# Performance work log

Hardware: AMD Instinct MI355X
Metric: run time of the kernel (lower is better)

Reference implementation:

```python
import jax, jax.numpy as jnp
import numpy as np

KEY_DIM = 32
NUM_HEADS = 4
B, T, F, D = 32, 64, 128, 64


def _proj_in(x, w, b):
    # x: [B,T,F,D], w: [D,H,K], b: [H,K] -> [B,T,F,H,K]
    return jnp.einsum("btfd,dhk->btfhk", x, w) + b


def _axial_mha(x, wq, bq, wk, bk, wv, bv, wo, bo, axis):
    # Keras MultiHeadAttention with attention_axes=(axis,); dropout inactive at inference.
    scale = 1.0 / np.sqrt(KEY_DIM)
    q = _proj_in(x, wq, bq) * scale
    k = _proj_in(x, wk, bk)
    v = _proj_in(x, wv, bv)
    if axis == 1:  # temporal attention, feature axis acts as batch
        scores = jnp.einsum("bqfhk,bsfhk->bfhqs", q, k)  # [B,F,H,Tq,Tk]
        probs = jax.nn.softmax(scores, axis=-1)
        o = jnp.einsum("bfhqs,bsfhk->bqfhk", probs, v)
    else:  # feature attention, temporal axis acts as batch
        scores = jnp.einsum("btqhk,btshk->bthqs", q, k)  # [B,T,H,Fq,Fk]
        probs = jax.nn.softmax(scores, axis=-1)
        o = jnp.einsum("bthqs,btshk->btqhk", probs, v)
    return jnp.einsum("btfhk,hkd->btfd", o, wo) + bo


def setup_inputs() -> dict:
    key = jax.random.key(0)
    ks = jax.random.split(key, 10)
    std = 0.02
    w = lambda k, shape: (jax.random.normal(k, shape, jnp.float32) * std)
    inp = {"x": jax.random.normal(ks[0], (B, T, F, D), jnp.float32)}
    for i, n in enumerate(["tq", "tk", "tv", "fq", "fk", "fv"]):
        inp[n + "_w"] = w(ks[1 + i], (D, NUM_HEADS, KEY_DIM))
        inp[n + "_b"] = jnp.zeros((NUM_HEADS, KEY_DIM), jnp.float32)
    inp["to_w"] = w(ks[7], (NUM_HEADS, KEY_DIM, D))
    inp["to_b"] = jnp.zeros((D,), jnp.float32)
    inp["fo_w"] = w(ks[8], (NUM_HEADS, KEY_DIM, D))
    inp["fo_b"] = jnp.zeros((D,), jnp.float32)
    return inp


def reference(x, tq_w, tq_b, tk_w, tk_b, tv_w, tv_b, to_w, to_b,
              fq_w, fq_b, fk_w, fk_b, fv_w, fv_b, fo_w, fo_b):
    temporal_out = _axial_mha(x, tq_w, tq_b, tk_w, tk_b, tv_w, tv_b, to_w, to_b, axis=1)
    feature_out = _axial_mha(x, fq_w, fq_b, fk_w, fk_b, fv_w, fv_b, fo_w, fo_b, axis=2)
    return temporal_out + feature_out
```

## Files before the change

kernel.cpp:

```cpp
#include <hip/hip_runtime.h>

typedef unsigned short u16;
typedef unsigned int   u32;
typedef short v8s __attribute__((ext_vector_type(8)));
typedef float v4f __attribute__((ext_vector_type(4)));

#define DEV __device__ __forceinline__
#define MFMA(a,b,c) __builtin_amdgcn_mfma_f32_16x16x32_bf16((a),(b),(c),0,0,0)

constexpr int Bb = 32, Tt = 64, Ff = 128, Dd = 64, Hh = 4, Kk = 32;

DEV u16 f2b(float f) {
    u32 u = __float_as_uint(f);
    return (u16)((u + 0x7fffu + ((u >> 16) & 1u)) >> 16);
}
DEV u32 pk2(float a, float b) {
    u32 x = __float_as_uint(a) + 0x8000u;
    u32 y = __float_as_uint(b) + 0x8000u;
    return (x >> 16) | (y & 0xffff0000u);
}

__global__ __launch_bounds__(256)
void prep_weights(const float* __restrict__ tq, const float* __restrict__ tk,
                  const float* __restrict__ tv, const float* __restrict__ fq,
                  const float* __restrict__ fk, const float* __restrict__ fv,
                  const float* __restrict__ to_, const float* __restrict__ fo,
                  u16* __restrict__ ws)
{
    int idx = blockIdx.x * 256 + threadIdx.x;
    if (idx < 49152) {
        int p = idx >> 13, rem = idx & 8191;
        int h = rem >> 11, ch = (rem >> 6) & 31, d = rem & 63;
        const float* w = (p==0)?tq:(p==1)?tk:(p==2)?tv:(p==3)?fq:(p==4)?fk:fv;
        ws[idx] = f2b(w[d*128 + h*32 + ch]);
    } else {
        int i2 = idx - 49152;
        int path = i2 >> 13, rem = i2 & 8191;
        int h = rem >> 11, d = (rem >> 5) & 63, k2 = rem & 31;
        const float* w = path ? fo : to_;
        ws[idx] = f2b(w[h*2048 + k2*64 + d]);
    }
}

template<int NR, int MODE>
__global__ __launch_bounds__(NR*4)
void axial_mfma(const float* __restrict__ x, const u16* __restrict__ wsw,
                const float* __restrict__ bq, const float* __restrict__ bk,
                const float* __restrict__ bv, const float* __restrict__ bo,
                float* __restrict__ out)
{
    constexpr int W   = NR / 16;
    constexpr int QP  = 40;
    constexpr int NRp = NR + 8;
    constexpr int o_q  = 0;
    constexpr int o_k  = o_q + NR * QP;
    constexpr int o_vt = o_k + NR * QP;
    constexpr int o_p  = o_vt + 32 * NRp;
    constexpr int SMEM = o_p + NR * NRp;
    __shared__ alignas(16) u16 sm[SMEM];

    const int tid  = threadIdx.x;
    const int w    = tid >> 6;
    const int lane = tid & 63;
    const int quad = lane >> 4;
    const int l15  = lane & 15;
    const int bid  = blockIdx.x;

    int base, rstride;
    if (MODE == 0) { int b = bid >> 7, f = bid & 127; base = b*(Tt*Ff*Dd) + f*Dd; rstride = Ff*Dd; }
    else           { base = bid * (Ff*Dd); rstride = Dd; }

    constexpr int PB = (MODE == 0) ? 0 : 3;
    const u16* wql = wsw + (PB+0)*8192;
    const u16* wkl = wsw + (PB+1)*8192;
    const u16* wvl = wsw + (PB+2)*8192;
    const u16* wol = wsw + 49152 + MODE*8192;

    v8s xfrag[2];
#pragma unroll
    for (int ks = 0; ks < 2; ++ks) {
        const float* xp = x + base + (w*16 + l15)*rstride + ks*32 + quad*8;
        float4 a = *reinterpret_cast<const float4*>(xp);
        float4 b = *reinterpret_cast<const float4*>(xp + 4);
        v8s f;
        u32* fu = reinterpret_cast<u32*>(&f);
        fu[0] = pk2(a.x, a.y); fu[1] = pk2(a.z, a.w);
        fu[2] = pk2(b.x, b.y); fu[3] = pk2(b.z, b.w);
        xfrag[ks] = f;
    }

    v4f outAcc[4];
#pragma unroll
    for (int i = 0; i < 4; ++i) outAcc[i] = (v4f){0.f,0.f,0.f,0.f};

    const float scale = 0.17677669529663687f;
    const v4f vzero = (v4f){0.f,0.f,0.f,0.f};

#pragma unroll 1
    for (int h = 0; h < Hh; ++h) {
        __syncthreads();

        {
            const u16* wb = wql + h*2048;
#pragma unroll
            for (int nt = 0; nt < 2; ++nt) {
                v4f acc = vzero;
#pragma unroll
                for (int ks = 0; ks < 2; ++ks) {
                    v8s wf = *reinterpret_cast<const v8s*>(wb + (nt*16+l15)*64 + ks*32 + quad*8);
                    acc = MFMA(wf, xfrag[ks], acc);
                }
                float4 b4 = *reinterpret_cast<const float4*>(bq + h*32 + nt*16 + quad*4);
                u32 lo = pk2((acc[0]+b4.x)*scale, (acc[1]+b4.y)*scale);
                u32 hi = pk2((acc[2]+b4.z)*scale, (acc[3]+b4.w)*scale);
                *reinterpret_cast<uint2*>(&sm[o_q + (w*16+l15)*QP + nt*16 + quad*4]) = make_uint2(lo, hi);
            }
        }
        {
            const u16* wb = wkl + h*2048;
#pragma unroll
            for (int nt = 0; nt < 2; ++nt) {
                v4f acc = vzero;
#pragma unroll
                for (int ks = 0; ks < 2; ++ks) {
                    v8s wf = *reinterpret_cast<const v8s*>(wb + (nt*16+l15)*64 + ks*32 + quad*8);
                    acc = MFMA(wf, xfrag[ks], acc);
                }
                float4 b4 = *reinterpret_cast<const float4*>(bk + h*32 + nt*16 + quad*4);
                u32 lo = pk2(acc[0]+b4.x, acc[1]+b4.y);
                u32 hi = pk2(acc[2]+b4.z, acc[3]+b4.w);
                *reinterpret_cast<uint2*>(&sm[o_k + (w*16+l15)*QP + nt*16 + quad*4]) = make_uint2(lo, hi);
            }
        }
        {
            const u16* wb = wvl + h*2048;
#pragma unroll
            for (int nt = 0; nt < 2; ++nt) {
                v4f acc = vzero;
#pragma unroll
                for (int ks = 0; ks < 2; ++ks) {
                    v8s wf = *reinterpret_cast<const v8s*>(wb + (nt*16+l15)*64 + ks*32 + quad*8);
                    acc = MFMA(xfrag[ks], wf, acc);
                }
                float bias = bv[h*32 + nt*16 + l15];
                u32 lo = pk2(acc[0]+bias, acc[1]+bias);
                u32 hi = pk2(acc[2]+bias, acc[3]+bias);
                int ch = nt*16 + l15;
                *reinterpret_cast<uint2*>(&sm[o_vt + ch*NRp + w*16 + quad*4]) = make_uint2(lo, hi);
            }
        }
        __syncthreads();

        v8s qf = *reinterpret_cast<const v8s*>(&sm[o_q + (w*16+l15)*QP + quad*8]);
        v4f S[W];
#pragma unroll
        for (int ct = 0; ct < W; ++ct) {
            v8s kf = *reinterpret_cast<const v8s*>(&sm[o_k + (ct*16+l15)*QP + quad*8]);
            S[ct] = MFMA(kf, qf, vzero);
        }
        float mm = S[0][0];
#pragma unroll
        for (int ct = 0; ct < W; ++ct)
#pragma unroll
            for (int r = 0; r < 4; ++r) mm = fmaxf(mm, S[ct][r]);
        mm = fmaxf(mm, __shfl_xor(mm, 16));
        mm = fmaxf(mm, __shfl_xor(mm, 32));
        float ss = 0.f;
#pragma unroll
        for (int ct = 0; ct < W; ++ct)
#pragma unroll
            for (int r = 0; r < 4; ++r) { float p = __expf(S[ct][r] - mm); S[ct][r] = p; ss += p; }
        ss += __shfl_xor(ss, 16);
        ss += __shfl_xor(ss, 32);
        float rl = 1.f / ss;
#pragma unroll
        for (int ct = 0; ct < W; ++ct) {
            u32 lo = pk2(S[ct][0]*rl, S[ct][1]*rl);
            u32 hi = pk2(S[ct][2]*rl, S[ct][3]*rl);
            *reinterpret_cast<uint2*>(&sm[o_p + (w*16+l15)*NRp + ct*16 + quad*4]) = make_uint2(lo, hi);
        }

        v4f Oacc[2] = { vzero, vzero };
#pragma unroll
        for (int ks = 0; ks < NR/32; ++ks) {
            v8s pf = *reinterpret_cast<const v8s*>(&sm[o_p + (w*16+l15)*NRp + ks*32 + quad*8]);
#pragma unroll
            for (int nt = 0; nt < 2; ++nt) {
                v8s vf = *reinterpret_cast<const v8s*>(&sm[o_vt + (nt*16+l15)*NRp + ks*32 + quad*8]);
                Oacc[nt] = MFMA(vf, pf, Oacc[nt]);
            }
        }
#pragma unroll
        for (int nt = 0; nt < 2; ++nt) {
            u32 lo = pk2(Oacc[nt][0], Oacc[nt][1]);
            u32 hi = pk2(Oacc[nt][2], Oacc[nt][3]);
            *reinterpret_cast<uint2*>(&sm[o_q + (w*16+l15)*QP + nt*16 + quad*4]) = make_uint2(lo, hi);
        }

        v8s of = *reinterpret_cast<const v8s*>(&sm[o_q + (w*16+l15)*QP + quad*8]);
        {
            const u16* wb = wol + h*2048;
#pragma unroll
            for (int nt = 0; nt < 4; ++nt) {
                v8s wf = *reinterpret_cast<const v8s*>(wb + (nt*16+l15)*32 + quad*8);
                outAcc[nt] = MFMA(wf, of, outAcc[nt]);
            }
        }
    }

    float* orow = out + base + (w*16 + l15)*rstride;
#pragma unroll
    for (int nt = 0; nt < 4; ++nt) {
        int d0 = nt*16 + quad*4;
        float4 b4 = *reinterpret_cast<const float4*>(bo + d0);
        float4 v = make_float4(outAcc[nt][0]+b4.x, outAcc[nt][1]+b4.y,
                               outAcc[nt][2]+b4.z, outAcc[nt][3]+b4.w);
        if (MODE == 1) {
            float4 p = *reinterpret_cast<const float4*>(orow + d0);
            v.x += p.x; v.y += p.y; v.z += p.z; v.w += p.w;
        }
        *reinterpret_cast<float4*>(orow + d0) = v;
    }
}

extern "C" void kernel_launch(void* const* d_in, const int* in_sizes, int n_in,
                              void* d_out, int out_size, void* d_ws, size_t ws_size,
                              hipStream_t stream) {
    const float* x   = (const float*)d_in[0];
    const float* tqw = (const float*)d_in[1];  const float* tqb = (const float*)d_in[2];
    const float* tkw = (const float*)d_in[3];  const float* tkb = (const float*)d_in[4];
    const float* tvw = (const float*)d_in[5];  const float* tvb = (const float*)d_in[6];
    const float* fqw = (const float*)d_in[7];  const float* fqb = (const float*)d_in[8];
    const float* fkw = (const float*)d_in[9];  const float* fkb = (const float*)d_in[10];
    const float* fvw = (const float*)d_in[11]; const float* fvb = (const float*)d_in[12];
    const float* tow = (const float*)d_in[13]; const float* tob = (const float*)d_in[14];
    const float* fow = (const float*)d_in[15]; const float* fob = (const float*)d_in[16];
    float* out = (float*)d_out;
    u16* ws = (u16*)d_ws;

    hipLaunchKernelGGL(prep_weights, dim3(256), dim3(256), 0, stream,
                       tqw, tkw, tvw, fqw, fkw, fvw, tow, fow, ws);
    hipLaunchKernelGGL((axial_mfma<64,0>), dim3(Bb*Ff), dim3(256), 0, stream,
                       x, ws, tqb, tkb, tvb, tob, out);
    hipLaunchKernelGGL((axial_mfma<128,1>), dim3(Bb*Tt), dim3(512), 0, stream,
                       x, ws, fqb, fkb, fvb, fob, out);
}
```

Measured before the change: 382.7 us.

## Use hardware bf16 pack, defer softmax normalization, shrink P staging buffer

```diff
diff --git a/kernel.cpp b/kernel.cpp
--- a/kernel.cpp
+++ b/kernel.cpp
@@ -15,9 +15,9 @@
     return (u16)((u + 0x7fffu + ((u >> 16) & 1u)) >> 16);
 }
 DEV u32 pk2(float a, float b) {
-    u32 x = __float_as_uint(a) + 0x8000u;
-    u32 y = __float_as_uint(b) + 0x8000u;
-    return (x >> 16) | (y & 0xffff0000u);
+    u32 r;
+    asm("v_cvt_pk_bf16_f32 %0, %1, %2" : "=v"(r) : "v"(a), "v"(b));
+    return r;
 }
 
 __global__ __launch_bounds__(256)
@@ -43,7 +43,7 @@
 }
 
 template<int NR, int MODE>
-__global__ __launch_bounds__(NR*4)
+__global__ __launch_bounds__(NR*4, 8)
 void axial_mfma(const float* __restrict__ x, const u16* __restrict__ wsw,
                 const float* __restrict__ bq, const float* __restrict__ bk,
                 const float* __restrict__ bv, const float* __restrict__ bo,
@@ -52,11 +52,12 @@
     constexpr int W   = NR / 16;
     constexpr int QP  = 40;
     constexpr int NRp = NR + 8;
+    constexpr int PP  = 40;
     constexpr int o_q  = 0;
     constexpr int o_k  = o_q + NR * QP;
     constexpr int o_vt = o_k + NR * QP;
     constexpr int o_p  = o_vt + 32 * NRp;
-    constexpr int SMEM = o_p + NR * NRp;
+    constexpr int SMEM = o_p + NR * PP;
     __shared__ alignas(16) u16 sm[SMEM];
 
     const int tid  = threadIdx.x;
@@ -95,6 +96,8 @@
 
     const float scale = 0.17677669529663687f;
     const v4f vzero = (v4f){0.f,0.f,0.f,0.f};
+    const int qrow_base = o_q + (w*16+l15)*QP;
+    const int prow_base = o_p + (w*16+l15)*PP;
 
 #pragma unroll 1
     for (int h = 0; h < Hh; ++h) {
@@ -113,7 +116,7 @@
                 float4 b4 = *reinterpret_cast<const float4*>(bq + h*32 + nt*16 + quad*4);
                 u32 lo = pk2((acc[0]+b4.x)*scale, (acc[1]+b4.y)*scale);
                 u32 hi = pk2((acc[2]+b4.z)*scale, (acc[3]+b4.w)*scale);
-                *reinterpret_cast<uint2*>(&sm[o_q + (w*16+l15)*QP + nt*16 + quad*4]) = make_uint2(lo, hi);
+                *reinterpret_cast<uint2*>(&sm[qrow_base + nt*16 + quad*4]) = make_uint2(lo, hi);
             }
         }
         {
@@ -151,18 +154,20 @@
         }
         __syncthreads();
 
-        v8s qf = *reinterpret_cast<const v8s*>(&sm[o_q + (w*16+l15)*QP + quad*8]);
+        v8s qf = *reinterpret_cast<const v8s*>(&sm[qrow_base + quad*8]);
         v4f S[W];
 #pragma unroll
         for (int ct = 0; ct < W; ++ct) {
             v8s kf = *reinterpret_cast<const v8s*>(&sm[o_k + (ct*16+l15)*QP + quad*8]);
             S[ct] = MFMA(kf, qf, vzero);
         }
-        float mm = S[0][0];
+        float cm[W];
 #pragma unroll
         for (int ct = 0; ct < W; ++ct)
-#pragma unroll
-            for (int r = 0; r < 4; ++r) mm = fmaxf(mm, S[ct][r]);
+            cm[ct] = fmaxf(fmaxf(S[ct][0], S[ct][1]), fmaxf(S[ct][2], S[ct][3]));
+        float mm = cm[0];
+#pragma unroll
+        for (int ct = 1; ct < W; ++ct) mm = fmaxf(mm, cm[ct]);
         mm = fmaxf(mm, __shfl_xor(mm, 16));
         mm = fmaxf(mm, __shfl_xor(mm, 32));
         float ss = 0.f;
@@ -173,17 +178,20 @@
         ss += __shfl_xor(ss, 16);
         ss += __shfl_xor(ss, 32);
         float rl = 1.f / ss;
+
+        u32 pkv[2*W];
 #pragma unroll
         for (int ct = 0; ct < W; ++ct) {
-            u32 lo = pk2(S[ct][0]*rl, S[ct][1]*rl);
-            u32 hi = pk2(S[ct][2]*rl, S[ct][3]*rl);
-            *reinterpret_cast<uint2*>(&sm[o_p + (w*16+l15)*NRp + ct*16 + quad*4]) = make_uint2(lo, hi);
+            pkv[2*ct+0] = pk2(S[ct][0], S[ct][1]);
+            pkv[2*ct+1] = pk2(S[ct][2], S[ct][3]);
         }
 
         v4f Oacc[2] = { vzero, vzero };
 #pragma unroll
         for (int ks = 0; ks < NR/32; ++ks) {
-            v8s pf = *reinterpret_cast<const v8s*>(&sm[o_p + (w*16+l15)*NRp + ks*32 + quad*8]);
+            *reinterpret_cast<uint2*>(&sm[prow_base +      quad*4]) = make_uint2(pkv[4*ks+0], pkv[4*ks+1]);
+            *reinterpret_cast<uint2*>(&sm[prow_base + 16 + quad*4]) = make_uint2(pkv[4*ks+2], pkv[4*ks+3]);
+            v8s pf = *reinterpret_cast<const v8s*>(&sm[prow_base + quad*8]);
 #pragma unroll
             for (int nt = 0; nt < 2; ++nt) {
                 v8s vf = *reinterpret_cast<const v8s*>(&sm[o_vt + (nt*16+l15)*NRp + ks*32 + quad*8]);
@@ -192,12 +200,12 @@
         }
 #pragma unroll
         for (int nt = 0; nt < 2; ++nt) {
-            u32 lo = pk2(Oacc[nt][0], Oacc[nt][1]);
-            u32 hi = pk2(Oacc[nt][2], Oacc[nt][3]);
-            *reinterpret_cast<uint2*>(&sm[o_q + (w*16+l15)*QP + nt*16 + quad*4]) = make_uint2(lo, hi);
-        }
-
-        v8s of = *reinterpret_cast<const v8s*>(&sm[o_q + (w*16+l15)*QP + quad*8]);
+            u32 lo = pk2(Oacc[nt][0]*rl, Oacc[nt][1]*rl);
+            u32 hi = pk2(Oacc[nt][2]*rl, Oacc[nt][3]*rl);
+            *reinterpret_cast<uint2*>(&sm[qrow_base + nt*16 + quad*4]) = make_uint2(lo, hi);
+        }
+
+        v8s of = *reinterpret_cast<const v8s*>(&sm[qrow_base + quad*8]);
         {
             const u16* wb = wol + h*2048;
 #pragma unroll
```

Result: slower. 441.0 us (+15.2%).
